# Performance work log

Measured on AMD Instinct MI355X. Metric: run time of the kernel, lower is better.

## Reference

```python
import jax, jax.numpy as jnp
import numpy as np

N_NODES = 100000
N_EDGES = 1600000
N_GRAPHS = 512
F_IN = 20
HID = 128
OUT = HID // 2


def _glorot(key, shape):
    fan_in, fan_out = shape[0], shape[1]
    lim = float(np.sqrt(6.0 / (fan_in + fan_out)))
    return jax.random.uniform(key, shape, jnp.float32, -lim, lim)


def setup_inputs() -> dict:
    key = jax.random.key(0)
    ks = jax.random.split(key, 12)
    x = jax.random.normal(ks[0], (N_NODES, F_IN), jnp.float32)
    edge_index = jax.random.randint(ks[1], (2, N_EDGES), 0, N_NODES, dtype=jnp.int64)
    batch = jnp.sort(jax.random.randint(ks[2], (N_NODES,), 0, N_GRAPHS, dtype=jnp.int64))
    return {
        "x": x,
        "edge_index": edge_index,
        "batch": batch,
        "W1": _glorot(ks[3], (F_IN, HID)), "b1": jnp.zeros((HID,), jnp.float32),
        "W2": _glorot(ks[4], (HID, HID)), "b2": jnp.zeros((HID,), jnp.float32),
        "W3": _glorot(ks[5], (HID, HID)), "b3": jnp.zeros((HID,), jnp.float32),
        "Wout": _glorot(ks[6], (HID, OUT)), "bout": jnp.zeros((OUT,), jnp.float32),
    }


def _gcn_conv(x, W, b, src, dst, num_nodes):
    # PyG GCNConv: x' = D^{-1/2} (A + I) D^{-1/2} X W + b (self-loops already in src/dst)
    xw = x @ W                                                  # [N, H]
    ones = jnp.ones(src.shape[0], dtype=xw.dtype)
    deg = jax.ops.segment_sum(ones, dst, num_segments=num_nodes)
    dinv = jnp.where(deg > 0, jax.lax.rsqrt(deg), 0.0)          # [N]
    norm = dinv[src] * dinv[dst]                                # [E+N]
    msg = xw[src] * norm[:, None]                               # gather + scale
    return jax.ops.segment_sum(msg, dst, num_segments=num_nodes) + b


def reference(x, edge_index, batch, W1, b1, W2, b2, W3, b3, Wout, bout):
    num_nodes = x.shape[0]
    loops = jnp.arange(num_nodes, dtype=edge_index.dtype)
    src = jnp.concatenate([edge_index[0], loops])
    dst = jnp.concatenate([edge_index[1], loops])

    h = jax.nn.relu(_gcn_conv(x, W1, b1, src, dst, num_nodes))
    h = jax.nn.relu(_gcn_conv(h, W2, b2, src, dst, num_nodes))
    h = jax.nn.relu(_gcn_conv(h, W3, b3, src, dst, num_nodes))

    # global_mean_pool over graph ids
    sums = jax.ops.segment_sum(h, batch, num_segments=N_GRAPHS)
    counts = jax.ops.segment_sum(jnp.ones(num_nodes, h.dtype), batch, num_segments=N_GRAPHS)
    pooled = sums / jnp.maximum(counts, 1.0)[:, None]           # [G, H]
    return pooled @ Wout + bout                                 # [G, H//2]
```

## Files before the change

kernel.cpp:

```cpp
#include <hip/hip_runtime.h>
#include <hip/hip_fp16.h>

#define N_NODES 100000
#define N_EDGES 1600000
#define N_GRAPHS 512
#define F_IN 20
#define HID 128
#define OUT_F 64

#define BUCKETS 256
#define SPAN 391
#define BCAP 7000
#define EPB 2048

typedef _Float16 half8_t __attribute__((ext_vector_type(8)));
typedef float f32x4_t __attribute__((ext_vector_type(4)));

__device__ inline float4 h4_to_f4(uint2 u) {
    __half2 h0 = *(__half2*)&u.x;
    __half2 h1 = *(__half2*)&u.y;
    float2 f0 = __half22float2(h0);
    float2 f1 = __half22float2(h1);
    return make_float4(f0.x, f0.y, f1.x, f1.y);
}

__global__ __launch_bounds__(256) void partition(const int* __restrict__ src,
                                                 const int* __restrict__ dst,
                                                 int* __restrict__ bpairs,
                                                 int* cur256) {
    __shared__ int lcnt[4][BUCKETS];
    __shared__ int woff[4][BUCKETS];
    int t = threadIdx.x;
    int wv = t >> 6;
    for (int i = t; i < 4 * BUCKETS; i += 256) ((int*)lcnt)[i] = 0;
    __syncthreads();
    int base = blockIdx.x * EPB;
    int myb[8], myp[8], myr[8];
#pragma unroll
    for (int i = 0; i < 8; ++i) {
        int e = base + i * 256 + t;
        int b = -1, p = 0, rk = 0;
        if (e < N_EDGES) {
            int s = src[e], d = dst[e];
            b = d / SPAN;
            p = (s << 9) | (d - b * SPAN);
            rk = atomicAdd(&lcnt[wv][b], 1);
        }
        myb[i] = b; myp[i] = p; myr[i] = rk;
    }
    __syncthreads();
    {
        int c0 = lcnt[0][t], c1 = lcnt[1][t], c2 = lcnt[2][t], c3 = lcnt[3][t];
        int gb = atomicAdd(&cur256[t], c0 + c1 + c2 + c3);
        woff[0][t] = gb;
        woff[1][t] = gb + c0;
        woff[2][t] = gb + c0 + c1;
        woff[3][t] = gb + c0 + c1 + c2;
    }
    __syncthreads();
#pragma unroll
    for (int i = 0; i < 8; ++i) {
        int b = myb[i];
        if (b >= 0) {
            int p = woff[wv][b] + myr[i];
            if (p < BCAP) bpairs[(size_t)b * BCAP + p] = myp[i];
        }
    }
}

__global__ void scan_bbase(const int* __restrict__ cur256, int* bbase, int* row_st) {
    __shared__ int sc[BUCKETS];
    int t = threadIdx.x;
    int v = cur256[t];
    sc[t] = v;
    __syncthreads();
    for (int o = 1; o < BUCKETS; o <<= 1) {
        int x = (t >= o) ? sc[t - o] : 0;
        __syncthreads();
        sc[t] += x;
        __syncthreads();
    }
    bbase[t] = sc[t] - v;
    if (t == 0) row_st[N_NODES] = N_EDGES;
}

__global__ __launch_bounds__(256) void csr_build(const int* __restrict__ bpairs,
                                                 const int* __restrict__ bcnt,
                                                 const int* __restrict__ bbase,
                                                 int* __restrict__ row_st,
                                                 int* __restrict__ csr) {
    __shared__ int ocnt[SPAN];
    __shared__ int sc[512];
    __shared__ int cur[SPAN];
    int b = blockIdx.x, t = threadIdx.x;
    int n0 = b * SPAN;
    int span = N_NODES - n0; if (span > SPAN) span = SPAN;
    for (int i = t; i < SPAN; i += 256) ocnt[i] = 0;
    __syncthreads();
    int n = bcnt[b];
    const int* p = bpairs + (size_t)b * BCAP;
    for (int i = t; i < n; i += 256) atomicAdd(&ocnt[p[i] & 511], 1);
    __syncthreads();
    sc[t]       = (t < span) ? ocnt[t] : 0;
    sc[t + 256] = (t + 256 < span) ? ocnt[t + 256] : 0;
    __syncthreads();
    for (int o = 1; o < 512; o <<= 1) {
        int a0 = (t >= o) ? sc[t - o] : 0;
        int a1 = sc[t + 256 - o];
        __syncthreads();
        sc[t] += a0;
        sc[t + 256] += a1;
        __syncthreads();
    }
    int base = bbase[b];
    for (int i = t; i < span; i += 256) {
        int start = sc[i] - ocnt[i];
        row_st[n0 + i] = base + start;
        cur[i] = start;
    }
    __syncthreads();
    for (int i = t; i < n; i += 256) {
        int e = p[i];
        int lp = atomicAdd(&cur[e & 511], 1);
        csr[base + lp] = e >> 9;
    }
}

__global__ void scale_x(const float* __restrict__ x, const int* __restrict__ row_st,
                        __half* __restrict__ Xs) {
    int i = blockIdx.x * 256 + threadIdx.x;
    int n = i >> 5, f = i & 31;
    if (n >= N_NODES) return;
    float v = (f < F_IN) ? x[n * F_IN + f] : 0.f;
    float di = rsqrtf((float)(row_st[n + 1] - row_st[n] + 1));
    Xs[i] = __float2half(di * v);
}

__global__ __launch_bounds__(256) void layer1(const __half* __restrict__ Xs,
                                              const int* __restrict__ row_st,
                                              const int* __restrict__ csr,
                                              const float* __restrict__ W,
                                              const float* __restrict__ bias,
                                              __half* __restrict__ H) {
    __shared__ float Wlds[F_IN * HID];
    __shared__ float Alds[16 * F_IN];
    const int t = threadIdx.x;
    const int node0 = blockIdx.x * 16;

    for (int i = t; i < F_IN * HID; i += 256) Wlds[i] = W[i];

    const int hw = t >> 5, l = t & 31;
    for (int k = 0; k < 2; ++k) {
        int nn = node0 + hw * 2 + k;
        int r0 = row_st[nn], r1 = row_st[nn + 1];
        float acc = __half2float(Xs[nn * 32 + l]);
        int r = r0;
        for (; r + 3 < r1; r += 4) {
            int s0 = csr[r], s1 = csr[r + 1], s2 = csr[r + 2], s3 = csr[r + 3];
            float v0 = __half2float(Xs[s0 * 32 + l]);
            float v1 = __half2float(Xs[s1 * 32 + l]);
            float v2 = __half2float(Xs[s2 * 32 + l]);
            float v3 = __half2float(Xs[s3 * 32 + l]);
            acc += (v0 + v1) + (v2 + v3);
        }
        for (; r < r1; ++r) acc += __half2float(Xs[csr[r] * 32 + l]);
        float di = rsqrtf((float)(r1 - r0 + 1));
        if (l < F_IN) Alds[(hw * 2 + k) * F_IN + l] = di * acc;
    }
    __syncthreads();

    const int h4 = (t & 31) * 4;
    const int g  = t >> 5;
    float4 b4 = *(const float4*)&bias[h4];
    float4 acc0 = b4;
    float4 acc1 = b4;
#pragma unroll
    for (int kk = 0; kk < F_IN; ++kk) {
        float a0 = Alds[(g * 2) * F_IN + kk];
        float a1 = Alds[(g * 2 + 1) * F_IN + kk];
        float4 w = *(const float4*)&Wlds[kk * HID + h4];
        acc0.x = fmaf(a0, w.x, acc0.x);
        acc0.y = fmaf(a0, w.y, acc0.y);
        acc0.z = fmaf(a0, w.z, acc0.z);
        acc0.w = fmaf(a0, w.w, acc0.w);
        acc1.x = fmaf(a1, w.x, acc1.x);
        acc1.y = fmaf(a1, w.y, acc1.y);
        acc1.z = fmaf(a1, w.z, acc1.z);
        acc1.w = fmaf(a1, w.w, acc1.w);
    }
    {
        __half2 h0 = __floats2half2_rn(acc0.x, acc0.y);
        __half2 h1 = __floats2half2_rn(acc0.z, acc0.w);
        uint2 u; u.x = *(unsigned*)&h0; u.y = *(unsigned*)&h1;
        ((uint2*)H)[(node0 + g * 2) * 32 + (h4 >> 2)] = u;
    }
    {
        __half2 h0 = __floats2half2_rn(acc1.x, acc1.y);
        __half2 h1 = __floats2half2_rn(acc1.z, acc1.w);
        uint2 u; u.x = *(unsigned*)&h0; u.y = *(unsigned*)&h1;
        ((uint2*)H)[(node0 + g * 2 + 1) * 32 + (h4 >> 2)] = u;
    }
}

__global__ __launch_bounds__(256) void gemm_mfma(const __half* __restrict__ H,
                                                 const float* __restrict__ W,
                                                 const int* __restrict__ row_st,
                                                 __half* __restrict__ T) {
    __shared__ _Float16 Whi[128 * 128];
    __shared__ _Float16 Wlo[128 * 128];
    const int t = threadIdx.x;

    for (int i = t; i < 128 * 128; i += 256) {
        int k = i >> 7, c = i & 127;
        float w = W[i];
        _Float16 hi = (_Float16)w;
        _Float16 lo = (_Float16)((w - (float)hi) * 2048.0f);
        int addr = c * 128 + (((k >> 3) ^ (c & 15)) << 3) + (k & 7);
        Whi[addr] = hi;
        Wlo[addr] = lo;
    }
    __syncthreads();

    const int wv = t >> 6;
    const int l  = t & 63;
    const int lr = l & 15;
    const int lq = l >> 4;

    for (int rep = 0; rep < 4; ++rep) {
        int strip = (blockIdx.x * 4 + wv) * 4 + rep;
        if (strip >= N_NODES / 16) continue;
        int n0 = strip * 16;

        f32x4_t acc[8], acl[8];
#pragma unroll
        for (int ct = 0; ct < 8; ++ct) { acc[ct] = (f32x4_t){0,0,0,0}; acl[ct] = (f32x4_t){0,0,0,0}; }

#pragma unroll
        for (int kc = 0; kc < 4; ++kc) {
            half8_t a = *(const half8_t*)(H + (size_t)(n0 + lr) * 128 + kc * 32 + lq * 8);
#pragma unroll
            for (int j = 0; j < 8; ++j) a[j] = a[j] > (_Float16)0 ? a[j] : (_Float16)0;
            int g = kc * 4 + lq;
#pragma unroll
            for (int ct = 0; ct < 8; ++ct) {
                int c = ct * 16 + lr;
                int addr = c * 128 + ((g ^ lr) << 3);
                half8_t bh = *(const half8_t*)&Whi[addr];
                half8_t bl = *(const half8_t*)&Wlo[addr];
                acc[ct] = __builtin_amdgcn_mfma_f32_16x16x32_f16(a, bh, acc[ct], 0, 0, 0);
                acl[ct] = __builtin_amdgcn_mfma_f32_16x16x32_f16(a, bl, acl[ct], 0, 0, 0);
            }
        }

        int r0 = n0 + lq * 4;
#pragma unroll
        for (int r = 0; r < 4; ++r) {
            int row = r0 + r;
            float d = rsqrtf((float)(row_st[row + 1] - row_st[row] + 1));
#pragma unroll
            for (int ct = 0; ct < 8; ++ct) {
                float v = (acc[ct][r] + acl[ct][r] * 4.8828125e-4f) * d;
                T[(size_t)row * 128 + ct * 16 + lr] = __float2half(v);
            }
        }
    }
}

__global__ __launch_bounds__(256) void gather_range(const __half* __restrict__ A,
                                                    const int* __restrict__ row_st,
                                                    const int* __restrict__ csr,
                                                    const float* __restrict__ bias,
                                                    __half* __restrict__ B) {
    int t = threadIdx.x;
    int n = blockIdx.x * 8 + (t >> 5);
    int l = t & 31;
    int r0 = row_st[n], r1 = row_st[n + 1];
    float di = rsqrtf((float)(r1 - r0 + 1));
    const uint2* Af = (const uint2*)A;
    float4 acc = h4_to_f4(Af[n * 32 + l]);
    int r = r0;
    for (; r + 7 < r1; r += 8) {
        int s0 = csr[r],     s1 = csr[r + 1], s2 = csr[r + 2], s3 = csr[r + 3];
        int s4 = csr[r + 4], s5 = csr[r + 5], s6 = csr[r + 6], s7 = csr[r + 7];
        float4 v0 = h4_to_f4(Af[s0 * 32 + l]);
        float4 v1 = h4_to_f4(Af[s1 * 32 + l]);
        float4 v2 = h4_to_f4(Af[s2 * 32 + l]);
        float4 v3 = h4_to_f4(Af[s3 * 32 + l]);
        float4 v4 = h4_to_f4(Af[s4 * 32 + l]);
        float4 v5 = h4_to_f4(Af[s5 * 32 + l]);
        float4 v6 = h4_to_f4(Af[s6 * 32 + l]);
        float4 v7 = h4_to_f4(Af[s7 * 32 + l]);
        acc.x += ((v0.x + v1.x) + (v2.x + v3.x)) + ((v4.x + v5.x) + (v6.x + v7.x));
        acc.y += ((v0.y + v1.y) + (v2.y + v3.y)) + ((v4.y + v5.y) + (v6.y + v7.y));
        acc.z += ((v0.z + v1.z) + (v2.z + v3.z)) + ((v4.z + v5.z) + (v6.z + v7.z));
        acc.w += ((v0.w + v1.w) + (v2.w + v3.w)) + ((v4.w + v5.w) + (v6.w + v7.w));
    }
    for (; r + 3 < r1; r += 4) {
        int s0 = csr[r], s1 = csr[r + 1], s2 = csr[r + 2], s3 = csr[r + 3];
        float4 v0 = h4_to_f4(Af[s0 * 32 + l]);
        float4 v1 = h4_to_f4(Af[s1 * 32 + l]);
        float4 v2 = h4_to_f4(Af[s2 * 32 + l]);
        float4 v3 = h4_to_f4(Af[s3 * 32 + l]);
        acc.x += (v0.x + v1.x) + (v2.x + v3.x);
        acc.y += (v0.y + v1.y) + (v2.y + v3.y);
        acc.z += (v0.z + v1.z) + (v2.z + v3.z);
        acc.w += (v0.w + v1.w) + (v2.w + v3.w);
    }
    for (; r < r1; ++r) {
        float4 v = h4_to_f4(Af[csr[r] * 32 + l]);
        acc.x += v.x; acc.y += v.y; acc.z += v.z; acc.w += v.w;
    }
    float4 b4 = ((const float4*)bias)[l];
    __half2 h0 = __floats2half2_rn(fmaf(di, acc.x, b4.x), fmaf(di, acc.y, b4.y));
    __half2 h1 = __floats2half2_rn(fmaf(di, acc.z, b4.z), fmaf(di, acc.w, b4.w));
    uint2 u; u.x = *(unsigned*)&h0; u.y = *(unsigned*)&h1;
    ((uint2*)B)[n * 32 + l] = u;
}

__global__ __launch_bounds__(256) void pool(const __half* __restrict__ B,
                                            const int* __restrict__ batch,
                                            float* sums, float* counts) {
    int t = threadIdx.x;
    int grp = blockIdx.x * 8 + (t >> 5);
    int l = t & 31;
    int h4 = l * 4;
    int n0 = grp * 8;
    if (n0 >= N_NODES) return;
    const uint2* Bf = (const uint2*)B;
    int cur = batch[n0];
    int runlen = 0;
    float4 acc = make_float4(0.f, 0.f, 0.f, 0.f);
    for (int k = 0; k < 8; ++k) {
        int n = n0 + k;
        if (n >= N_NODES) break;
        int g = batch[n];
        if (g != cur) {
            float* sp = &sums[cur * HID + h4];
            atomicAdd(sp + 0, acc.x); atomicAdd(sp + 1, acc.y);
            atomicAdd(sp + 2, acc.z); atomicAdd(sp + 3, acc.w);
            if (l == 0) atomicAdd(&counts[cur], (float)runlen);
            acc = make_float4(0.f, 0.f, 0.f, 0.f);
            runlen = 0;
            cur = g;
        }
        float4 v = h4_to_f4(Bf[n * 32 + l]);
        acc.x += fmaxf(v.x, 0.f);
        acc.y += fmaxf(v.y, 0.f);
        acc.z += fmaxf(v.z, 0.f);
        acc.w += fmaxf(v.w, 0.f);
        ++runlen;
    }
    float* sp = &sums[cur * HID + h4];
    atomicAdd(sp + 0, acc.x); atomicAdd(sp + 1, acc.y);
    atomicAdd(sp + 2, acc.z); atomicAdd(sp + 3, acc.w);
    if (l == 0) atomicAdd(&counts[cur], (float)runlen);
}

__global__ void final_gemm(const float* __restrict__ sums, const float* __restrict__ counts,
                           const float* __restrict__ Wout, const float* __restrict__ bout,
                           float* __restrict__ out) {
    int g = blockIdx.x;
    int o = threadIdx.x;
    __shared__ float p[HID];
    for (int k = o; k < HID; k += 64) p[k] = sums[g * HID + k];
    __syncthreads();
    float inv = 1.0f / fmaxf(counts[g], 1.0f);
    float acc = 0.f;
#pragma unroll 8
    for (int k = 0; k < HID; ++k)
        acc = fmaf(p[k], Wout[k * OUT_F + o], acc);
    out[g * OUT_F + o] = fmaf(inv, acc, bout[o]);
}

extern "C" void kernel_launch(void* const* d_in, const int* in_sizes, int n_in,
                              void* d_out, int out_size, void* d_ws, size_t ws_size,
                              hipStream_t stream) {
    const float* x     = (const float*)d_in[0];
    const int*   ei    = (const int*)d_in[1];
    const int*   batch = (const int*)d_in[2];
    const float* W1    = (const float*)d_in[3];
    const float* b1    = (const float*)d_in[4];
    const float* W2    = (const float*)d_in[5];
    const float* b2    = (const float*)d_in[6];
    const float* W3    = (const float*)d_in[7];
    const float* b3    = (const float*)d_in[8];
    const float* Wout  = (const float*)d_in[9];
    const float* bout  = (const float*)d_in[10];
    float* out = (float*)d_out;

    const int* src = ei;
    const int* dst = ei + N_EDGES;

    float* A      = (float*)d_ws;
    float* Breg   = A + (size_t)N_NODES * HID;
    int*   row_st = (int*)(Breg + (size_t)N_NODES * HID);
    float* sums   = (float*)(row_st + N_NODES + 1);
    float* counts = sums + N_GRAPHS * HID;
    int*   csr    = (int*)(counts + N_GRAPHS);
    int*   cur256 = csr + N_EDGES;
    int*   bbase  = cur256 + BUCKETS;

    int*    bpairs = (int*)A;
    __half* Xs     = (__half*)A;
    __half* T      = (__half*)A;
    __half* H      = (__half*)Breg;

    hipMemsetAsync(sums, 0, (N_GRAPHS * HID + N_GRAPHS) * sizeof(float), stream);
    hipMemsetAsync(cur256, 0, BUCKETS * sizeof(int), stream);
    partition<<<(N_EDGES + EPB - 1) / EPB, 256, 0, stream>>>(src, dst, bpairs, cur256);
    scan_bbase<<<1, BUCKETS, 0, stream>>>(cur256, bbase, row_st);
    csr_build<<<BUCKETS, 256, 0, stream>>>(bpairs, cur256, bbase, row_st, csr);

    scale_x<<<N_NODES * 32 / 256, 256, 0, stream>>>(x, row_st, Xs);
    layer1<<<N_NODES / 16, 256, 0, stream>>>(Xs, row_st, csr, W1, b1, H);

    gemm_mfma<<<391, 256, 0, stream>>>(H, W2, row_st, T);
    gather_range<<<N_NODES / 8, 256, 0, stream>>>(T, row_st, csr, b2, H);
    gemm_mfma<<<391, 256, 0, stream>>>(H, W3, row_st, T);
    gather_range<<<N_NODES / 8, 256, 0, stream>>>(T, row_st, csr, b3, H);

    pool<<<(N_NODES / 8 + 7) / 8, 256, 0, stream>>>(H, batch, sums, counts);
    final_gemm<<<N_GRAPHS, 64, 0, stream>>>(sums, counts, Wout, bout, out);
}
```

Before: 411.7 us.

## Fuse scan and x-scaling into csr_build, split gemm columns, vectorize layer1 gather

The bucket-base scan moves into each csr_build block, and the scale_x kernel is folded into csr_build using the local degree counts, which removes two launches and a memset. layer1's gather now reads half2 pairs, with two half-warps splitting the edges and merging through a shuffle. gemm_mfma splits the 128 output columns across two blocks, halving LDS per block and doubling the grid to raise occupancy, at the cost of reading each H strip twice. Xs is placed at an offset so it does not overlap bpairs, since both are now live in the same kernel.

New measurement: 405.1 us. About the same (-1.6%).

```diff
diff --git a/kernel.cpp b/kernel.cpp
--- a/kernel.cpp
+++ b/kernel.cpp
@@ -68,36 +68,36 @@
     }
 }
 
-__global__ void scan_bbase(const int* __restrict__ cur256, int* bbase, int* row_st) {
-    __shared__ int sc[BUCKETS];
-    int t = threadIdx.x;
-    int v = cur256[t];
-    sc[t] = v;
-    __syncthreads();
-    for (int o = 1; o < BUCKETS; o <<= 1) {
-        int x = (t >= o) ? sc[t - o] : 0;
-        __syncthreads();
-        sc[t] += x;
-        __syncthreads();
-    }
-    bbase[t] = sc[t] - v;
-    if (t == 0) row_st[N_NODES] = N_EDGES;
-}
-
 __global__ __launch_bounds__(256) void csr_build(const int* __restrict__ bpairs,
-                                                 const int* __restrict__ bcnt,
-                                                 const int* __restrict__ bbase,
+                                                 const int* __restrict__ cur256,
                                                  int* __restrict__ row_st,
-                                                 int* __restrict__ csr) {
+                                                 int* __restrict__ csr,
+                                                 const float* __restrict__ x,
+                                                 __half* __restrict__ Xs) {
     __shared__ int ocnt[SPAN];
     __shared__ int sc[512];
     __shared__ int cur[SPAN];
+    __shared__ int sbase;
     int b = blockIdx.x, t = threadIdx.x;
+
+    int myc = cur256[t];
+    sc[t] = myc;
+    __syncthreads();
+    for (int o = 1; o < BUCKETS; o <<= 1) {
+        int v = (t >= o) ? sc[t - o] : 0;
+        __syncthreads();
+        sc[t] += v;
+        __syncthreads();
+    }
+    if (t == b) sbase = sc[t] - myc;
+    if (b == BUCKETS - 1 && t == 0) row_st[N_NODES] = N_EDGES;
+
     int n0 = b * SPAN;
     int span = N_NODES - n0; if (span > SPAN) span = SPAN;
     for (int i = t; i < SPAN; i += 256) ocnt[i] = 0;
     __syncthreads();
-    int n = bcnt[b];
+
+    int n = cur256[b];
     const int* p = bpairs + (size_t)b * BCAP;
     for (int i = t; i < n; i += 256) atomicAdd(&ocnt[p[i] & 511], 1);
     __syncthreads();
@@ -112,7 +112,7 @@
         sc[t + 256] += a1;
         __syncthreads();
     }
-    int base = bbase[b];
+    int base = sbase;
     for (int i = t; i < span; i += 256) {
         int start = sc[i] - ocnt[i];
         row_st[n0 + i] = base + start;
@@ -124,16 +124,12 @@
         int lp = atomicAdd(&cur[e & 511], 1);
         csr[base + lp] = e >> 9;
     }
-}
-
-__global__ void scale_x(const float* __restrict__ x, const int* __restrict__ row_st,
-                        __half* __restrict__ Xs) {
-    int i = blockIdx.x * 256 + threadIdx.x;
-    int n = i >> 5, f = i & 31;
-    if (n >= N_NODES) return;
-    float v = (f < F_IN) ? x[n * F_IN + f] : 0.f;
-    float di = rsqrtf((float)(row_st[n + 1] - row_st[n] + 1));
-    Xs[i] = __float2half(di * v);
+    for (int i = t; i < span * 32; i += 256) {
+        int nl = i >> 5, f = i & 31;
+        float v = (f < F_IN) ? x[(size_t)(n0 + nl) * F_IN + f] : 0.f;
+        float di = rsqrtf((float)(ocnt[nl] + 1));
+        Xs[(size_t)(n0 + nl) * 32 + f] = __float2half(di * v);
+    }
 }
 
 __global__ __launch_bounds__(256) void layer1(const __half* __restrict__ Xs,
@@ -149,28 +145,40 @@
 
     for (int i = t; i < F_IN * HID; i += 256) Wlds[i] = W[i];
 
-    const int hw = t >> 5, l = t & 31;
-    for (int k = 0; k < 2; ++k) {
-        int nn = node0 + hw * 2 + k;
+    const int g = t >> 5;
+    const int l = t & 31;
+    const int hw = l >> 4, l16 = l & 15;
+    const __half2* X2 = (const __half2*)Xs;
+    for (int k2 = 0; k2 < 2; ++k2) {
+        int nn = node0 + g * 2 + k2;
         int r0 = row_st[nn], r1 = row_st[nn + 1];
-        float acc = __half2float(Xs[nn * 32 + l]);
-        int r = r0;
-        for (; r + 3 < r1; r += 4) {
-            int s0 = csr[r], s1 = csr[r + 1], s2 = csr[r + 2], s3 = csr[r + 3];
-            float v0 = __half2float(Xs[s0 * 32 + l]);
-            float v1 = __half2float(Xs[s1 * 32 + l]);
-            float v2 = __half2float(Xs[s2 * 32 + l]);
-            float v3 = __half2float(Xs[s3 * 32 + l]);
-            acc += (v0 + v1) + (v2 + v3);
-        }
-        for (; r < r1; ++r) acc += __half2float(Xs[csr[r] * 32 + l]);
-        float di = rsqrtf((float)(r1 - r0 + 1));
-        if (l < F_IN) Alds[(hw * 2 + k) * F_IN + l] = di * acc;
+        float2 acc = make_float2(0.f, 0.f);
+        if (hw == 0) {
+            float2 f = __half22float2(X2[(size_t)nn * 16 + l16]);
+            acc = f;
+        }
+        int r = r0 + hw;
+        for (; r + 2 < r1; r += 4) {
+            float2 f0 = __half22float2(X2[(size_t)csr[r] * 16 + l16]);
+            float2 f1 = __half22float2(X2[(size_t)csr[r + 2] * 16 + l16]);
+            acc.x += f0.x + f1.x;
+            acc.y += f0.y + f1.y;
+        }
+        if (r < r1) {
+            float2 f = __half22float2(X2[(size_t)csr[r] * 16 + l16]);
+            acc.x += f.x; acc.y += f.y;
+        }
+        acc.x += __shfl_xor(acc.x, 16);
+        acc.y += __shfl_xor(acc.y, 16);
+        if (hw == 0 && l16 < 10) {
+            float di = rsqrtf((float)(r1 - r0 + 1));
+            Alds[(g * 2 + k2) * F_IN + l16 * 2]     = di * acc.x;
+            Alds[(g * 2 + k2) * F_IN + l16 * 2 + 1] = di * acc.y;
+        }
     }
     __syncthreads();
 
     const int h4 = (t & 31) * 4;
-    const int g  = t >> 5;
     float4 b4 = *(const float4*)&bias[h4];
     float4 acc0 = b4;
     float4 acc1 = b4;
@@ -206,13 +214,14 @@
                                                  const float* __restrict__ W,
                                                  const int* __restrict__ row_st,
                                                  __half* __restrict__ T) {
-    __shared__ _Float16 Whi[128 * 128];
-    __shared__ _Float16 Wlo[128 * 128];
+    __shared__ _Float16 Whi[64 * 128];
+    __shared__ _Float16 Wlo[64 * 128];
     const int t = threadIdx.x;
-
-    for (int i = t; i < 128 * 128; i += 256) {
-        int k = i >> 7, c = i & 127;
-        float w = W[i];
+    const int c0 = (blockIdx.x & 1) * 64;
+
+    for (int i = t; i < 128 * 64; i += 256) {
+        int k = i >> 6, c = i & 63;
+        float w = W[k * HID + c0 + c];
         _Float16 hi = (_Float16)w;
         _Float16 lo = (_Float16)((w - (float)hi) * 2048.0f);
         int addr = c * 128 + (((k >> 3) ^ (c & 15)) << 3) + (k & 7);
@@ -227,13 +236,13 @@
     const int lq = l >> 4;
 
     for (int rep = 0; rep < 4; ++rep) {
-        int strip = (blockIdx.x * 4 + wv) * 4 + rep;
+        int strip = ((blockIdx.x >> 1) * 4 + wv) * 4 + rep;
         if (strip >= N_NODES / 16) continue;
         int n0 = strip * 16;
 
-        f32x4_t acc[8], acl[8];
-#pragma unroll
-        for (int ct = 0; ct < 8; ++ct) { acc[ct] = (f32x4_t){0,0,0,0}; acl[ct] = (f32x4_t){0,0,0,0}; }
+        f32x4_t acc[4], acl[4];
+#pragma unroll
+        for (int ct = 0; ct < 4; ++ct) { acc[ct] = (f32x4_t){0,0,0,0}; acl[ct] = (f32x4_t){0,0,0,0}; }
 
 #pragma unroll
         for (int kc = 0; kc < 4; ++kc) {
@@ -242,7 +251,7 @@
             for (int j = 0; j < 8; ++j) a[j] = a[j] > (_Float16)0 ? a[j] : (_Float16)0;
             int g = kc * 4 + lq;
 #pragma unroll
-            for (int ct = 0; ct < 8; ++ct) {
+            for (int ct = 0; ct < 4; ++ct) {
                 int c = ct * 16 + lr;
                 int addr = c * 128 + ((g ^ lr) << 3);
                 half8_t bh = *(const half8_t*)&Whi[addr];
@@ -258,9 +267,9 @@
             int row = r0 + r;
             float d = rsqrtf((float)(row_st[row + 1] - row_st[row] + 1));
 #pragma unroll
-            for (int ct = 0; ct < 8; ++ct) {
+            for (int ct = 0; ct < 4; ++ct) {
                 float v = (acc[ct][r] + acl[ct][r] * 4.8828125e-4f) * d;
-                T[(size_t)row * 128 + ct * 16 + lr] = __float2half(v);
+                T[(size_t)row * 128 + c0 + ct * 16 + lr] = __float2half(v);
             }
         }
     }
@@ -396,27 +405,23 @@
     int*   row_st = (int*)(Breg + (size_t)N_NODES * HID);
     float* sums   = (float*)(row_st + N_NODES + 1);
     float* counts = sums + N_GRAPHS * HID;
-    int*   csr    = (int*)(counts + N_GRAPHS);
-    int*   cur256 = csr + N_EDGES;
-    int*   bbase  = cur256 + BUCKETS;
+    int*   cur256 = (int*)(counts + N_GRAPHS);
+    int*   csr    = cur256 + BUCKETS;
 
     int*    bpairs = (int*)A;
-    __half* Xs     = (__half*)A;
+    __half* Xs     = (__half*)((char*)A + 7168000);
     __half* T      = (__half*)A;
     __half* H      = (__half*)Breg;
 
-    hipMemsetAsync(sums, 0, (N_GRAPHS * HID + N_GRAPHS) * sizeof(float), stream);
-    hipMemsetAsync(cur256, 0, BUCKETS * sizeof(int), stream);
+    hipMemsetAsync(sums, 0, (size_t)(N_GRAPHS * HID + N_GRAPHS + BUCKETS) * 4, stream);
     partition<<<(N_EDGES + EPB - 1) / EPB, 256, 0, stream>>>(src, dst, bpairs, cur256);
-    scan_bbase<<<1, BUCKETS, 0, stream>>>(cur256, bbase, row_st);
-    csr_build<<<BUCKETS, 256, 0, stream>>>(bpairs, cur256, bbase, row_st, csr);
-
-    scale_x<<<N_NODES * 32 / 256, 256, 0, stream>>>(x, row_st, Xs);
+    csr_build<<<BUCKETS, 256, 0, stream>>>(bpairs, cur256, row_st, csr, x, Xs);
+
     layer1<<<N_NODES / 16, 256, 0, stream>>>(Xs, row_st, csr, W1, b1, H);
 
-    gemm_mfma<<<391, 256, 0, stream>>>(H, W2, row_st, T);
+    gemm_mfma<<<782, 256, 0, stream>>>(H, W2, row_st, T);
     gather_range<<<N_NODES / 8, 256, 0, stream>>>(T, row_st, csr, b2, H);
-    gemm_mfma<<<391, 256, 0, stream>>>(H, W3, row_st, T);
+    gemm_mfma<<<782, 256, 0, stream>>>(H, W3, row_st, T);
     gather_range<<<N_NODES / 8, 256, 0, stream>>>(T, row_st, csr, b3, H);
 
     pool<<<(N_NODES / 8 + 7) / 8, 256, 0, stream>>>(H, batch, sums, counts);
```
